# Performance work log

Measured on AMD Instinct MI355X. Metric: run time of the kernel, lower is better.

Reference implementation:

```python
import jax, jax.numpy as jnp
import numpy as np
import math

D_MODEL = 1024
NUM_HEADS = 16
HEAD_DIM = D_MODEL // NUM_HEADS
THETA = 10000.0
B, S = 2, 2048


def apply_rope(x, pos, theta=THETA):
    # x: [..., S, D]; pos: [S] int. Rotates consecutive (even, odd) pairs.
    d = x.shape[-1]
    inv_freq = theta ** (-jnp.arange(0, d, 2, dtype=jnp.float32) / d)  # [d/2]
    ang = pos.astype(jnp.float32)[:, None] * inv_freq[None, :]          # [S, d/2]
    cos, sin = jnp.cos(ang), jnp.sin(ang)
    xe = x[..., 0::2]
    xo = x[..., 1::2]
    re = xe * cos - xo * sin
    ro = xe * sin + xo * cos
    return jnp.stack([re, ro], axis=-1).reshape(x.shape)


def setup_inputs() -> dict:
    key = jax.random.key(0)
    ks = jax.random.split(key, 5)
    scale = 1.0 / math.sqrt(D_MODEL)
    return {
        "in_features": jax.random.normal(ks[0], (B, S, D_MODEL), dtype=jnp.float32),
        "token_positions": jnp.arange(S, dtype=jnp.int32),
        "wq": jax.random.normal(ks[1], (D_MODEL, D_MODEL), dtype=jnp.float32) * scale,
        "wk": jax.random.normal(ks[2], (D_MODEL, D_MODEL), dtype=jnp.float32) * scale,
        "wv": jax.random.normal(ks[3], (D_MODEL, D_MODEL), dtype=jnp.float32) * scale,
        "wo": jax.random.normal(ks[4], (D_MODEL, D_MODEL), dtype=jnp.float32) * scale,
    }


def reference(in_features, token_positions, wq, wk, wv, wo):
    x = in_features
    b, s, d = x.shape
    # Linear: y = x @ W.T  (weight stored as [out, in])
    def split_heads(y):
        return y.reshape(b, s, NUM_HEADS, HEAD_DIM).transpose(0, 2, 1, 3)  # [B,H,S,Dh]
    Q = split_heads(x @ wq.T)
    K = split_heads(x @ wk.T)
    V = split_heads(x @ wv.T)
    Q = apply_rope(Q, token_positions)
    K = apply_rope(K, token_positions)
    scores = jnp.einsum('bhqd,bhkd->bhqk', Q, K) / math.sqrt(HEAD_DIM)
    causal = jnp.tril(jnp.ones((s, s), dtype=bool))
    scores = jnp.where(causal, scores, -jnp.inf)
    weights = jax.nn.softmax(scores, axis=-1)
    out = jnp.einsum('bhqk,bhkd->bhqd', weights, V)  # [B,H,S,Dh]
    out = out.transpose(0, 2, 1, 3).reshape(b, s, d)
    return out @ wo.T
```

## Files before the change

### kernel.cpp

```cpp
#include <hip/hip_runtime.h>
#include <hip/hip_bf16.h>

typedef __bf16 bf16_t;
typedef __bf16 bf16x8 __attribute__((ext_vector_type(8)));
typedef __bf16 bf16x4 __attribute__((ext_vector_type(4)));
typedef float  f32x4  __attribute__((ext_vector_type(4)));
typedef float  f32x16 __attribute__((ext_vector_type(16)));
typedef unsigned int u32;
typedef unsigned int u32x2v __attribute__((ext_vector_type(2)));
typedef unsigned int u32x4v __attribute__((ext_vector_type(4)));

#define D_MODEL   1024
#define NQKV      3072
#define NUM_HEADS 16
#define HEAD_DIM  64
#define SEQ       2048
#define BATCH     2
#define NTOK      4096
#define SM_SCALE_LOG2E 0.18033688011112042f
#define NEG_BIG  (-3.0e38f)

__device__ __forceinline__ int swz128(int row, int bytecol) {
  return row*128 + ((((bytecol>>4) ^ (row&7))<<4) | (bytecol & 15));
}

__device__ __forceinline__ void gload16(const void* g, void* l) {
  __builtin_amdgcn_global_load_lds((const __attribute__((address_space(1))) u32*)g,
                                   (__attribute__((address_space(3))) u32*)l, 16, 0, 0);
}

__device__ __forceinline__ u32 cvtpk_bf16(float a, float b) {
  u32 r;
  asm("v_cvt_pk_bf16_f32 %0, %1, %2" : "=v"(r) : "v"(a), "v"(b));
  return r;
}

__device__ __forceinline__ void plswap(u32 &a, u32 &b) {
#if __has_builtin(__builtin_amdgcn_permlane32_swap)
  u32x2v r = __builtin_amdgcn_permlane32_swap(a, b, false, false);
  a = r[0]; b = r[1];
#else
  u32 xa = __shfl_xor((unsigned)a, 32, 64);
  u32 xb = __shfl_xor((unsigned)b, 32, 64);
  bool hi = (threadIdx.x & 32) != 0;
  a = hi ? xb : a;
  b = hi ? b : xa;
#endif
}

__device__ const unsigned char slot_order96[96] = {
  30,31,88,90,92,93,94,95,
  28,29,80,82,84,85,86,87,89,91,
  26,27,72,74,76,77,78,79,81,83,
  24,25,64,66,68,69,70,71,73,75,
  22,23,56,58,60,61,62,63,65,67,
  20,21,48,50,52,53,54,55,57,59,
  18,19,40,42,44,45,46,47,49,51,
  16,17,32,34,36,37,38,39,41,43,
  14,15,33,35,
  12,13, 10,11, 8,9, 6,7, 4,5, 2,3, 0,1
};

__global__ void cvt_x(const float* __restrict__ in, bf16_t* __restrict__ out) {
  int i = (blockIdx.x*256 + threadIdx.x)*4;
  float4 v = *reinterpret_cast<const float4*>(in + i);
  bf16x4 o; o[0]=(bf16_t)v.x; o[1]=(bf16_t)v.y; o[2]=(bf16_t)v.z; o[3]=(bf16_t)v.w;
  *reinterpret_cast<bf16x4*>(out + i) = o;
}

__global__ void cvt_w(const float* __restrict__ wq, const float* __restrict__ wk,
                      const float* __restrict__ wv, const float* __restrict__ wo,
                      bf16_t* __restrict__ wqkv, bf16_t* __restrict__ wob) {
  const int NW = D_MODEL*D_MODEL;
  int i = (blockIdx.x*256 + threadIdx.x)*4;
  float4 v;
  if      (i <   NW) v = *reinterpret_cast<const float4*>(wq + i);
  else if (i < 2*NW) v = *reinterpret_cast<const float4*>(wk + i - NW);
  else if (i < 3*NW) v = *reinterpret_cast<const float4*>(wv + i - 2*NW);
  else               v = *reinterpret_cast<const float4*>(wo + i - 3*NW);
  bf16x4 o; o[0]=(bf16_t)v.x; o[1]=(bf16_t)v.y; o[2]=(bf16_t)v.z; o[3]=(bf16_t)v.w;
  bf16_t* dst = (i < 3*NW) ? (wqkv + i) : (wob + i - 3*NW);
  *reinterpret_cast<bf16x4*>(dst) = o;
}

__global__ void rope_qk(bf16_t* __restrict__ QKV, const int* __restrict__ pos) {
  int i = blockIdx.x*256 + threadIdx.x;
  int j = i & 31;
  int hp = (i >> 5) & 15;
  int t  = i >> 9;
  float ang = (float)pos[t & (SEQ-1)] * exp2f(-(float)j * (13.287712379549449f/32.0f));
  float sv, cv; sincosf(ang, &sv, &cv);
  size_t base = (size_t)t*NQKV + hp*64 + 2*j;
  float xe = (float)QKV[base], xo = (float)QKV[base+1];
  QKV[base]   = (bf16_t)((xe*cv - xo*sv)*SM_SCALE_LOG2E);
  QKV[base+1] = (bf16_t)((xe*sv + xo*cv)*SM_SCALE_LOG2E);
  xe = (float)QKV[base+1024]; xo = (float)QKV[base+1025];
  QKV[base+1024] = (bf16_t)(xe*cv - xo*sv);
  QKV[base+1025] = (bf16_t)(xe*sv + xo*cv);
}

template<typename OutT, bool QKV>
__global__ __launch_bounds__(256, 1) void gemm8(const bf16_t* __restrict__ A,
                                                const bf16_t* __restrict__ B,
                                                OutT* __restrict__ C,
                                                bf16_t* __restrict__ Vt,
                                                int M, int N, int K) {
  __shared__ __align__(16) char lds[4][32768];
  int tid = threadIdx.x;
  int n0 = blockIdx.x*128, m0 = blockIdx.y*128;
  int wid = tid>>6, lane = tid&63;
  int wr = wid>>1, wc = wid&1;
  int lr = lane&15, lg = lane>>4;

  const int nT = K >> 6;

  int srow = tid >> 3;
  int sc8  = (tid & 7) ^ (srow & 7);
  const bf16_t* ga = A + (size_t)(m0 + srow)*K + sc8*8;
  const bf16_t* gb = B + (size_t)(n0 + srow)*K + sc8*8;

  f32x4 acc[4][4];
  #pragma unroll
  for (int a=0;a<4;a++)
    #pragma unroll
    for (int b=0;b<4;b++) acc[a][b] = (f32x4){0.f,0.f,0.f,0.f};

  auto stage = [&](int t) {
    char* s = lds[t&3];
    int k0 = t << 6;
    #pragma unroll
    for (int g=0; g<4; g++)
      gload16(ga + (size_t)(g*32)*K + k0, s + g*4096 + tid*16);
    #pragma unroll
    for (int g=0; g<4; g++)
      gload16(gb + (size_t)(g*32)*K + k0, s + 16384 + g*4096 + tid*16);
  };

  stage(0);
  if (nT > 1) stage(1);
  asm volatile("s_waitcnt vmcnt(8)" ::: "memory");
  __builtin_amdgcn_sched_barrier(0);
  __builtin_amdgcn_s_barrier();

  for (int t = 0; t < nT; ++t) {
    char* sA = lds[t&3];
    char* sB = sA + 16384;

    bf16x8 bq[4][2], aq[2][2];
    #pragma unroll
    for (int ni=0; ni<4; ni++)
      #pragma unroll
      for (int ks=0; ks<2; ks++)
        bq[ni][ks] = *reinterpret_cast<const bf16x8*>(sB + swz128(wc*64+ni*16+lr, ks*64+lg*16));
    #pragma unroll
    for (int mi=0; mi<2; mi++)
      #pragma unroll
      for (int ks=0; ks<2; ks++)
        aq[mi][ks] = *reinterpret_cast<const bf16x8*>(sA + swz128(wr*64+mi*16+lr, ks*64+lg*16));
    if (t + 2 < nT) stage(t + 2);
    asm volatile("s_waitcnt lgkmcnt(0)" ::: "memory");
    __builtin_amdgcn_sched_barrier(0);
    __builtin_amdgcn_s_setprio(1);
    #pragma unroll
    for (int mi=0; mi<2; mi++)
      #pragma unroll
      for (int ni=0; ni<4; ni++)
        #pragma unroll
        for (int ks=0; ks<2; ks++)
          acc[mi][ni] = __builtin_amdgcn_mfma_f32_16x16x32_bf16(aq[mi][ks], bq[ni][ks], acc[mi][ni], 0, 0, 0);
    __builtin_amdgcn_s_setprio(0);
    __builtin_amdgcn_s_barrier();

    bf16x8 aq2[2][2];
    #pragma unroll
    for (int mi=0; mi<2; mi++)
      #pragma unroll
      for (int ks=0; ks<2; ks++)
        aq2[mi][ks] = *reinterpret_cast<const bf16x8*>(sA + swz128(wr*64+(mi+2)*16+lr, ks*64+lg*16));
    asm volatile("s_waitcnt lgkmcnt(0)" ::: "memory");
    __builtin_amdgcn_sched_barrier(0);
    __builtin_amdgcn_s_setprio(1);
    #pragma unroll
    for (int mi=0; mi<2; mi++)
      #pragma unroll
      for (int ni=0; ni<4; ni++)
        #pragma unroll
        for (int ks=0; ks<2; ks++)
          acc[mi+2][ni] = __builtin_amdgcn_mfma_f32_16x16x32_bf16(aq2[mi][ks], bq[ni][ks], acc[mi+2][ni], 0, 0, 0);
    __builtin_amdgcn_s_setprio(0);
    if (t + 2 < nT)      { asm volatile("s_waitcnt vmcnt(8)" ::: "memory"); }
    else if (t + 1 < nT) { asm volatile("s_waitcnt vmcnt(0)" ::: "memory"); }
    __builtin_amdgcn_sched_barrier(0);
    __builtin_amdgcn_s_barrier();
  }

  if (!QKV || n0 < 2*D_MODEL) {
    #pragma unroll
    for (int mi=0;mi<4;mi++)
      #pragma unroll
      for (int ni=0;ni<4;ni++)
        #pragma unroll
        for (int r=0;r<4;r++) {
          int m = m0 + wr*64 + mi*16 + lg*4 + r;
          int n = n0 + wc*64 + ni*16 + lr;
          C[(size_t)m*N + n] = (OutT)acc[mi][ni][r];
        }
  } else {
    #pragma unroll
    for (int mi=0;mi<4;mi++)
      #pragma unroll
      for (int ni=0;ni<4;ni++)
        #pragma unroll
        for (int r=0;r<4;r++) {
          int m = m0 + wr*64 + mi*16 + lg*4 + r;
          int nl = n0 + wc*64 + ni*16 + lr - 2*D_MODEL;
          int h = nl >> 6, d = nl & 63;
          int bb = m >> 11, s = m & (SEQ-1);
          Vt[(((size_t)(bb*16 + h)*64 + d) << 11) + s] = (bf16_t)acc[mi][ni][r];
        }
  }
}

__global__ __launch_bounds__(64, 3) void attn10(const bf16_t* __restrict__ QKV,
                                                const bf16_t* __restrict__ Vt,
                                                bf16_t* __restrict__ pO,
                                                float2* __restrict__ pML) {
  __shared__ __align__(16) char sK[64*128];

  int bh = blockIdx.x;
  int b = bh >> 4, h = bh & 15;
  int lane = threadIdx.x & 63;
  int q32 = lane & 31, hi = lane >> 5;
  int rsub = lane >> 3, sg = (lane & 7) ^ rsub;

  int s = slot_order96[blockIdx.y];
  int qw, t0, t1;
  if (s < 32) { qw = s; t0 = 0; t1 = (s >> 1) + 1; }
  else {
    int e = s - 32;
    qw = 32 + (e >> 1);
    int nt = (qw >> 1) + 1, h0 = (nt + 1) >> 1;
    t0 = (e & 1) ? h0 : 0;
    t1 = (e & 1) ? nt : h0;
  }
  int qt   = qw >> 1;
  int slot = bh*96 + s;
  int qg   = qw*32 + q32;

  bf16x8 qf[4];
  const bf16_t* qrow = QKV + (size_t)(b*SEQ + qw*32 + q32)*NQKV + h*64 + hi*8;
  #pragma unroll
  for (int d=0; d<4; d++) qf[d] = *reinterpret_cast<const bf16x8*>(qrow + d*16);

  const bf16_t* kgb = QKV + D_MODEL + ((size_t)(b*SEQ) + rsub)*NQKV + h*64 + sg*8;
  const bf16_t* vg0 = Vt + (size_t)bh*64*SEQ + (size_t)q32*SEQ + hi*8;
  const bf16_t* vg1 = vg0 + (size_t)32*SEQ;

  auto stageK = [&](int t) {
    const bf16_t* src = kgb + (size_t)t*64*NQKV;
    #pragma unroll
    for (int c=0;c<8;c++)
      gload16(src + (size_t)(8*c)*NQKV, sK + c*1024 + lane*16);
  };

  f32x16 O0 = (f32x16)0.0f, O1 = (f32x16)0.0f;
  float mrun = NEG_BIG, lrun = 0.f;

  stageK(t0);
  asm volatile("s_waitcnt vmcnt(0)" ::: "memory");
  __builtin_amdgcn_sched_barrier(0);

  for (int ti = t0; ti < t1; ++ti) {
    bf16x8 k0f[4], k1f[4];
    #pragma unroll
    for (int ds=0; ds<4; ds++) {
      k0f[ds] = *reinterpret_cast<const bf16x8*>(sK + swz128(q32,    ds*32 + hi*16));
      k1f[ds] = *reinterpret_cast<const bf16x8*>(sK + swz128(32+q32, ds*32 + hi*16));
    }
    bf16x8 v0f[4], v1f[4];
    #pragma unroll
    for (int ks=0; ks<4; ks++) {
      v0f[ks] = *reinterpret_cast<const bf16x8*>(vg0 + ti*64 + ks*16);
      v1f[ks] = *reinterpret_cast<const bf16x8*>(vg1 + ti*64 + ks*16);
    }
    asm volatile("s_waitcnt lgkmcnt(0)" ::: "memory");
    __builtin_amdgcn_sched_barrier(0);
    if (ti + 1 < t1) stageK(ti + 1);

    f32x16 p0 = (f32x16)0.0f, p1 = (f32x16)0.0f;
    __builtin_amdgcn_s_setprio(1);
    #pragma unroll
    for (int ds=0; ds<4; ds++) {
      p0 = __builtin_amdgcn_mfma_f32_32x32x16_bf16(k0f[ds], qf[ds], p0, 0, 0, 0);
      p1 = __builtin_amdgcn_mfma_f32_32x32x16_bf16(k1f[ds], qf[ds], p1, 0, 0, 0);
    }
    __builtin_amdgcn_s_setprio(0);

    if (ti == qt) {
      #pragma unroll
      for (int r=0; r<16; r++) {
        int kg = ti*64 + (r&3) + 8*(r>>2) + 4*hi;
        if (kg      > qg) p0[r] = NEG_BIG;
        if (kg + 32 > qg) p1[r] = NEG_BIG;
      }
    }

    float mx[8];
    #pragma unroll
    for (int r=0;r<8;r++) mx[r] = fmaxf(fmaxf(p0[r],p0[r+8]), fmaxf(p1[r],p1[r+8]));
    #pragma unroll
    for (int st=4; st>0; st>>=1)
      #pragma unroll
      for (int r=0;r<st;r++) mx[r] = fmaxf(mx[r], mx[r+st]);
    float mt = fmaxf(mx[0], __shfl_xor(mx[0], 32, 64));

    if (!__all(mt <= mrun + 8.0f)) {
      float mnew  = fmaxf(mrun, mt);
      float alpha = exp2f(mrun - mnew);
      lrun *= alpha;
      O0 *= alpha; O1 *= alpha;
      mrun = mnew;
    }
    #pragma unroll
    for (int r=0; r<16; r++) {
      p0[r] = exp2f(p0[r] - mrun);
      p1[r] = exp2f(p1[r] - mrun);
    }
    float sx[8];
    #pragma unroll
    for (int r=0;r<8;r++) sx[r] = (p0[r]+p0[r+8]) + (p1[r]+p1[r+8]);
    #pragma unroll
    for (int st=4; st>0; st>>=1)
      #pragma unroll
      for (int r=0;r<st;r++) sx[r] += sx[r+st];
    lrun += sx[0] + __shfl_xor(sx[0], 32, 64);

    u32 pk0[8], pk1[8];
    #pragma unroll
    for (int i2=0; i2<8; i2++) {
      pk0[i2] = cvtpk_bf16(p0[2*i2], p0[2*i2+1]);
      pk1[i2] = cvtpk_bf16(p1[2*i2], p1[2*i2+1]);
    }
    plswap(pk0[0], pk0[2]); plswap(pk0[1], pk0[3]);
    plswap(pk0[4], pk0[6]); plswap(pk0[5], pk0[7]);
    plswap(pk1[0], pk1[2]); plswap(pk1[1], pk1[3]);
    plswap(pk1[4], pk1[6]); plswap(pk1[5], pk1[7]);

    bf16x8 pa[4];
    pa[0] = __builtin_bit_cast(bf16x8, (u32x4v){pk0[0],pk0[1],pk0[2],pk0[3]});
    pa[1] = __builtin_bit_cast(bf16x8, (u32x4v){pk0[4],pk0[5],pk0[6],pk0[7]});
    pa[2] = __builtin_bit_cast(bf16x8, (u32x4v){pk1[0],pk1[1],pk1[2],pk1[3]});
    pa[3] = __builtin_bit_cast(bf16x8, (u32x4v){pk1[4],pk1[5],pk1[6],pk1[7]});

    __builtin_amdgcn_s_setprio(1);
    #pragma unroll
    for (int ks=0; ks<4; ks++) {
      O0 = __builtin_amdgcn_mfma_f32_32x32x16_bf16(v0f[ks], pa[ks], O0, 0, 0, 0);
      O1 = __builtin_amdgcn_mfma_f32_32x32x16_bf16(v1f[ks], pa[ks], O1, 0, 0, 0);
    }
    __builtin_amdgcn_s_setprio(0);

    if (ti + 1 < t1) {
      asm volatile("s_waitcnt vmcnt(0)" ::: "memory");
      __builtin_amdgcn_sched_barrier(0);
    }
  }

  bf16_t* prow = pO + ((size_t)slot*2048 + q32*64);
  #pragma unroll
  for (int rg=0; rg<4; rg++) {
    int d0 = 8*rg + 4*hi;
    u32 a0 = cvtpk_bf16(O0[4*rg],   O0[4*rg+1]);
    u32 a1 = cvtpk_bf16(O0[4*rg+2], O0[4*rg+3]);
    *reinterpret_cast<u32x2v*>(prow + d0) = (u32x2v){a0, a1};
    u32 b0 = cvtpk_bf16(O1[4*rg],   O1[4*rg+1]);
    u32 b1 = cvtpk_bf16(O1[4*rg+2], O1[4*rg+3]);
    *reinterpret_cast<u32x2v*>(prow + 32 + d0) = (u32x2v){b0, b1};
  }
  if (hi == 0)
    pML[slot*32 + q32] = make_float2(mrun, lrun);
}

__global__ __launch_bounds__(128) void combine(const bf16_t* __restrict__ pO,
                                               const float2* __restrict__ pML,
                                               bf16_t* __restrict__ Of) {
  int qw = blockIdx.x, bh = blockIdx.y;
  int b = bh >> 4, h = bh & 15;
  int t = threadIdx.x;
  int q = t >> 2, d0 = (t & 3) * 16;
  bf16x8 r0, r1;
  if (qw < 32) {
    int slot = bh*96 + qw;
    float2 ml = pML[slot*32 + q];
    float inv = 1.0f / ml.y;
    const bf16x8* src = reinterpret_cast<const bf16x8*>(pO + (size_t)slot*2048 + q*64 + d0);
    bf16x8 o0 = src[0], o1 = src[1];
    #pragma unroll
    for (int i=0;i<8;i++) {
      r0[i] = (bf16_t)((float)o0[i]*inv);
      r1[i] = (bf16_t)((float)o1[i]*inv);
    }
  } else {
    int s0 = bh*96 + 32 + (qw-32)*2;
    float2 mlA = pML[s0*32 + q];
    float2 mlB = pML[(s0+1)*32 + q];
    float m  = fmaxf(mlA.x, mlB.x);
    float a0 = exp2f(mlA.x - m), a1 = exp2f(mlB.x - m);
    float inv = 1.0f / (a0*mlA.y + a1*mlB.y);
    a0 *= inv; a1 *= inv;
    const bf16x8* sA = reinterpret_cast<const bf16x8*>(pO + (size_t)s0*2048 + q*64 + d0);
    const bf16x8* sB = reinterpret_cast<const bf16x8*>(pO + (size_t)(s0+1)*2048 + q*64 + d0);
    bf16x8 oa0 = sA[0], oa1 = sA[1], ob0 = sB[0], ob1 = sB[1];
    #pragma unroll
    for (int i=0;i<8;i++) {
      r0[i] = (bf16_t)(a0*(float)oa0[i] + a1*(float)ob0[i]);
      r1[i] = (bf16_t)(a0*(float)oa1[i] + a1*(float)ob1[i]);
    }
  }
  bf16x8* dst = reinterpret_cast<bf16x8*>(Of + ((size_t)(b*SEQ) + qw*32 + q)*D_MODEL + h*64 + d0);
  dst[0] = r0; dst[1] = r1;
}

extern "C" void kernel_launch(void* const* d_in, const int* in_sizes, int n_in,
                              void* d_out, int out_size, void* d_ws, size_t ws_size,
                              hipStream_t stream) {
  const float* x   = (const float*)d_in[0];
  const int*   pos = (const int*)  d_in[1];
  const float* wq  = (const float*)d_in[2];
  const float* wk  = (const float*)d_in[3];
  const float* wv  = (const float*)d_in[4];
  const float* wo  = (const float*)d_in[5];
  float* out = (float*)d_out;

  char* ws = (char*)d_ws;
  bf16_t* xb   = (bf16_t*)(ws);
  bf16_t* wqkv = (bf16_t*)(ws + ( 8u<<20));
  bf16_t* wob  = (bf16_t*)(ws + (14u<<20));
  bf16_t* QKV  = (bf16_t*)(ws + (16u<<20));
  bf16_t* Vtb  = (bf16_t*)(ws + (40u<<20));
  bf16_t* pO   = (bf16_t*)(ws);
  float2* pML  = (float2*)(ws + (13u<<20));
  bf16_t* Of   = (bf16_t*)(ws + (40u<<20));

  cvt_x<<<NTOK*D_MODEL/1024, 256, 0, stream>>>(x, xb);
  cvt_w<<<4*D_MODEL*D_MODEL/1024, 256, 0, stream>>>(wq, wk, wv, wo, wqkv, wob);

  dim3 gqkv(NQKV/128, NTOK/128);
  gemm8<bf16_t, true><<<gqkv, 256, 0, stream>>>(xb, wqkv, QKV, Vtb, NTOK, NQKV, D_MODEL);

  rope_qk<<<NTOK*NUM_HEADS*32/256, 256, 0, stream>>>(QKV, pos);

  dim3 gattn(32, 96);
  attn10<<<gattn, 64, 0, stream>>>(QKV, Vtb, pO, pML);

  dim3 gcomb(64, 32);
  combine<<<gcomb, 128, 0, stream>>>(pO, pML, Of);

  dim3 gout(D_MODEL/128, NTOK/128);
  gemm8<float, false><<<gout, 256, 0, stream>>>(Of, wob, out, nullptr, NTOK, D_MODEL, D_MODEL);
}
```

Baseline: 136.9 us.

## Double KV tile to 128 keys and stage V through swizzled LDS

```diff
diff --git a/kernel.cpp b/kernel.cpp
--- a/kernel.cpp
+++ b/kernel.cpp
@@ -22,6 +22,9 @@
 
 __device__ __forceinline__ int swz128(int row, int bytecol) {
   return row*128 + ((((bytecol>>4) ^ (row&7))<<4) | (bytecol & 15));
+}
+__device__ __forceinline__ int swz256(int row, int bytecol) {
+  return row*256 + ((((bytecol>>4) ^ (row&15))<<4) | (bytecol & 15));
 }
 
 __device__ __forceinline__ void gload16(const void* g, void* l) {
@@ -49,16 +52,12 @@
 }
 
 __device__ const unsigned char slot_order96[96] = {
-  30,31,88,90,92,93,94,95,
-  28,29,80,82,84,85,86,87,89,91,
-  26,27,72,74,76,77,78,79,81,83,
-  24,25,64,66,68,69,70,71,73,75,
-  22,23,56,58,60,61,62,63,65,67,
-  20,21,48,50,52,53,54,55,57,59,
-  18,19,40,42,44,45,46,47,49,51,
-  16,17,32,34,36,37,38,39,41,43,
-  14,15,33,35,
-  12,13, 10,11, 8,9, 6,7, 4,5, 2,3, 0,1
+  28,29,30,31, 80,82,84,86, 88,89,90,91,92,93,94,95,
+  24,25,26,27, 64,66,68,70, 72,73,74,75,76,77,78,79, 81,83,85,87,
+  20,21,22,23, 48,50,52,54, 56,57,58,59,60,61,62,63, 65,67,69,71,
+  16,17,18,19, 32,34,36,38, 40,41,42,43,44,45,46,47, 49,51,53,55,
+  12,13,14,15, 33,35,37,39,
+  8,9,10,11, 4,5,6,7, 0,1,2,3
 };
 
 __global__ void cvt_x(const float* __restrict__ in, bf16_t* __restrict__ out) {
@@ -221,11 +220,12 @@
   }
 }
 
-__global__ __launch_bounds__(64, 3) void attn10(const bf16_t* __restrict__ QKV,
+__global__ __launch_bounds__(64, 2) void attn12(const bf16_t* __restrict__ QKV,
                                                 const bf16_t* __restrict__ Vt,
                                                 bf16_t* __restrict__ pO,
                                                 float2* __restrict__ pML) {
-  __shared__ __align__(16) char sK[64*128];
+  __shared__ __align__(16) char sK[128*128];
+  __shared__ __align__(16) char sV[64*256];
 
   int bh = blockIdx.x;
   int b = bh >> 4, h = bh & 15;
@@ -235,15 +235,15 @@
 
   int s = slot_order96[blockIdx.y];
   int qw, t0, t1;
-  if (s < 32) { qw = s; t0 = 0; t1 = (s >> 1) + 1; }
+  if (s < 32) { qw = s; t0 = 0; t1 = (s >> 2) + 1; }
   else {
     int e = s - 32;
     qw = 32 + (e >> 1);
-    int nt = (qw >> 1) + 1, h0 = (nt + 1) >> 1;
+    int nt = (qw >> 2) + 1, h0 = (nt + 1) >> 1;
     t0 = (e & 1) ? h0 : 0;
     t1 = (e & 1) ? nt : h0;
   }
-  int qt   = qw >> 1;
+  int qt   = qw >> 2;
   int slot = bh*96 + s;
   int qg   = qw*32 + q32;
 
@@ -253,61 +253,70 @@
   for (int d=0; d<4; d++) qf[d] = *reinterpret_cast<const bf16x8*>(qrow + d*16);
 
   const bf16_t* kgb = QKV + D_MODEL + ((size_t)(b*SEQ) + rsub)*NQKV + h*64 + sg*8;
-  const bf16_t* vg0 = Vt + (size_t)bh*64*SEQ + (size_t)q32*SEQ + hi*8;
-  const bf16_t* vg1 = vg0 + (size_t)32*SEQ;
+  const bf16_t* Vb  = Vt + (size_t)bh*64*SEQ;
 
   auto stageK = [&](int t) {
-    const bf16_t* src = kgb + (size_t)t*64*NQKV;
-    #pragma unroll
-    for (int c=0;c<8;c++)
+    const bf16_t* src = kgb + (size_t)t*128*NQKV;
+    #pragma unroll
+    for (int c=0;c<16;c++)
       gload16(src + (size_t)(8*c)*NQKV, sK + c*1024 + lane*16);
   };
+  auto stageV = [&](int t) {
+    #pragma unroll
+    for (int c=0;c<16;c++) {
+      int row = 4*c + (lane>>4);
+      int sgv = (lane&15) ^ (row & 15);
+      gload16(Vb + (size_t)row*SEQ + t*128 + sgv*8, sV + c*1024 + lane*16);
+    }
+  };
 
   f32x16 O0 = (f32x16)0.0f, O1 = (f32x16)0.0f;
   float mrun = NEG_BIG, lrun = 0.f;
 
-  stageK(t0);
-  asm volatile("s_waitcnt vmcnt(0)" ::: "memory");
-  __builtin_amdgcn_sched_barrier(0);
+  stageK(t0); stageV(t0);
 
   for (int ti = t0; ti < t1; ++ti) {
-    bf16x8 k0f[4], k1f[4];
-    #pragma unroll
-    for (int ds=0; ds<4; ds++) {
-      k0f[ds] = *reinterpret_cast<const bf16x8*>(sK + swz128(q32,    ds*32 + hi*16));
-      k1f[ds] = *reinterpret_cast<const bf16x8*>(sK + swz128(32+q32, ds*32 + hi*16));
-    }
-    bf16x8 v0f[4], v1f[4];
-    #pragma unroll
-    for (int ks=0; ks<4; ks++) {
-      v0f[ks] = *reinterpret_cast<const bf16x8*>(vg0 + ti*64 + ks*16);
-      v1f[ks] = *reinterpret_cast<const bf16x8*>(vg1 + ti*64 + ks*16);
-    }
+    asm volatile("s_waitcnt vmcnt(16)" ::: "memory");
+    __builtin_amdgcn_sched_barrier(0);
+
+    f32x16 p0 = (f32x16)0.0f, p1 = (f32x16)0.0f;
+    f32x16 p2 = (f32x16)0.0f, p3 = (f32x16)0.0f;
+    __builtin_amdgcn_s_setprio(1);
+    #pragma unroll
+    for (int g=0; g<4; g++) {
+      bf16x8 kf[4];
+      #pragma unroll
+      for (int ds=0; ds<4; ds++)
+        kf[ds] = *reinterpret_cast<const bf16x8*>(sK + swz128(g*32 + q32, ds*32 + hi*16));
+      #pragma unroll
+      for (int ds=0; ds<4; ds++) {
+        if (g == 0) p0 = __builtin_amdgcn_mfma_f32_32x32x16_bf16(kf[ds], qf[ds], p0, 0, 0, 0);
+        if (g == 1) p1 = __builtin_amdgcn_mfma_f32_32x32x16_bf16(kf[ds], qf[ds], p1, 0, 0, 0);
+        if (g == 2) p2 = __builtin_amdgcn_mfma_f32_32x32x16_bf16(kf[ds], qf[ds], p2, 0, 0, 0);
+        if (g == 3) p3 = __builtin_amdgcn_mfma_f32_32x32x16_bf16(kf[ds], qf[ds], p3, 0, 0, 0);
+      }
+    }
+    __builtin_amdgcn_s_setprio(0);
     asm volatile("s_waitcnt lgkmcnt(0)" ::: "memory");
     __builtin_amdgcn_sched_barrier(0);
     if (ti + 1 < t1) stageK(ti + 1);
 
-    f32x16 p0 = (f32x16)0.0f, p1 = (f32x16)0.0f;
-    __builtin_amdgcn_s_setprio(1);
-    #pragma unroll
-    for (int ds=0; ds<4; ds++) {
-      p0 = __builtin_amdgcn_mfma_f32_32x32x16_bf16(k0f[ds], qf[ds], p0, 0, 0, 0);
-      p1 = __builtin_amdgcn_mfma_f32_32x32x16_bf16(k1f[ds], qf[ds], p1, 0, 0, 0);
-    }
-    __builtin_amdgcn_s_setprio(0);
-
     if (ti == qt) {
       #pragma unroll
       for (int r=0; r<16; r++) {
-        int kg = ti*64 + (r&3) + 8*(r>>2) + 4*hi;
-        if (kg      > qg) p0[r] = NEG_BIG;
-        if (kg + 32 > qg) p1[r] = NEG_BIG;
+        int kg = ti*128 + (r&3) + 8*(r>>2) + 4*hi;
+        if (kg       > qg) p0[r] = NEG_BIG;
+        if (kg + 32  > qg) p1[r] = NEG_BIG;
+        if (kg + 64  > qg) p2[r] = NEG_BIG;
+        if (kg + 96  > qg) p3[r] = NEG_BIG;
       }
     }
 
     float mx[8];
     #pragma unroll
-    for (int r=0;r<8;r++) mx[r] = fmaxf(fmaxf(p0[r],p0[r+8]), fmaxf(p1[r],p1[r+8]));
+    for (int r=0;r<8;r++)
+      mx[r] = fmaxf(fmaxf(fmaxf(p0[r],p0[r+8]), fmaxf(p1[r],p1[r+8])),
+                    fmaxf(fmaxf(p2[r],p2[r+8]), fmaxf(p3[r],p3[r+8])));
     #pragma unroll
     for (int st=4; st>0; st>>=1)
       #pragma unroll
@@ -325,45 +334,56 @@
     for (int r=0; r<16; r++) {
       p0[r] = exp2f(p0[r] - mrun);
       p1[r] = exp2f(p1[r] - mrun);
+      p2[r] = exp2f(p2[r] - mrun);
+      p3[r] = exp2f(p3[r] - mrun);
     }
     float sx[8];
     #pragma unroll
-    for (int r=0;r<8;r++) sx[r] = (p0[r]+p0[r+8]) + (p1[r]+p1[r+8]);
+    for (int r=0;r<8;r++)
+      sx[r] = ((p0[r]+p0[r+8]) + (p1[r]+p1[r+8])) + ((p2[r]+p2[r+8]) + (p3[r]+p3[r+8]));
     #pragma unroll
     for (int st=4; st>0; st>>=1)
       #pragma unroll
       for (int r=0;r<st;r++) sx[r] += sx[r+st];
     lrun += sx[0] + __shfl_xor(sx[0], 32, 64);
 
-    u32 pk0[8], pk1[8];
-    #pragma unroll
-    for (int i2=0; i2<8; i2++) {
-      pk0[i2] = cvtpk_bf16(p0[2*i2], p0[2*i2+1]);
-      pk1[i2] = cvtpk_bf16(p1[2*i2], p1[2*i2+1]);
-    }
-    plswap(pk0[0], pk0[2]); plswap(pk0[1], pk0[3]);
-    plswap(pk0[4], pk0[6]); plswap(pk0[5], pk0[7]);
-    plswap(pk1[0], pk1[2]); plswap(pk1[1], pk1[3]);
-    plswap(pk1[4], pk1[6]); plswap(pk1[5], pk1[7]);
-
-    bf16x8 pa[4];
-    pa[0] = __builtin_bit_cast(bf16x8, (u32x4v){pk0[0],pk0[1],pk0[2],pk0[3]});
-    pa[1] = __builtin_bit_cast(bf16x8, (u32x4v){pk0[4],pk0[5],pk0[6],pk0[7]});
-    pa[2] = __builtin_bit_cast(bf16x8, (u32x4v){pk1[0],pk1[1],pk1[2],pk1[3]});
-    pa[3] = __builtin_bit_cast(bf16x8, (u32x4v){pk1[4],pk1[5],pk1[6],pk1[7]});
+    bf16x8 pa[8];
+    #pragma unroll
+    for (int g=0; g<4; g++) {
+      u32 pk[8];
+      #pragma unroll
+      for (int i2=0; i2<8; i2++) {
+        float a = (g==0)?p0[2*i2]:(g==1)?p1[2*i2]:(g==2)?p2[2*i2]:p3[2*i2];
+        float c = (g==0)?p0[2*i2+1]:(g==1)?p1[2*i2+1]:(g==2)?p2[2*i2+1]:p3[2*i2+1];
+        pk[i2] = cvtpk_bf16(a, c);
+      }
+      plswap(pk[0], pk[2]); plswap(pk[1], pk[3]);
+      plswap(pk[4], pk[6]); plswap(pk[5], pk[7]);
+      pa[2*g]   = __builtin_bit_cast(bf16x8, (u32x4v){pk[0],pk[1],pk[2],pk[3]});
+      pa[2*g+1] = __builtin_bit_cast(bf16x8, (u32x4v){pk[4],pk[5],pk[6],pk[7]});
+    }
+
+    if (ti + 1 < t1) { asm volatile("s_waitcnt vmcnt(16)" ::: "memory"); }
+    else             { asm volatile("s_waitcnt vmcnt(0)"  ::: "memory"); }
+    __builtin_amdgcn_sched_barrier(0);
+
+    bf16x8 v0f[8], v1f[8];
+    #pragma unroll
+    for (int ks=0; ks<8; ks++) {
+      v0f[ks] = *reinterpret_cast<const bf16x8*>(sV + swz256(q32,    ks*32 + hi*16));
+      v1f[ks] = *reinterpret_cast<const bf16x8*>(sV + swz256(32+q32, ks*32 + hi*16));
+    }
+    asm volatile("s_waitcnt lgkmcnt(0)" ::: "memory");
+    __builtin_amdgcn_sched_barrier(0);
+    if (ti + 1 < t1) stageV(ti + 1);
 
     __builtin_amdgcn_s_setprio(1);
     #pragma unroll
-    for (int ks=0; ks<4; ks++) {
+    for (int ks=0; ks<8; ks++) {
       O0 = __builtin_amdgcn_mfma_f32_32x32x16_bf16(v0f[ks], pa[ks], O0, 0, 0, 0);
       O1 = __builtin_amdgcn_mfma_f32_32x32x16_bf16(v1f[ks], pa[ks], O1, 0, 0, 0);
     }
     __builtin_amdgcn_s_setprio(0);
-
-    if (ti + 1 < t1) {
-      asm volatile("s_waitcnt vmcnt(0)" ::: "memory");
-      __builtin_amdgcn_sched_barrier(0);
-    }
   }
 
   bf16_t* prow = pO + ((size_t)slot*2048 + q32*64);
@@ -451,7 +471,7 @@
   rope_qk<<<NTOK*NUM_HEADS*32/256, 256, 0, stream>>>(QKV, pos);
 
   dim3 gattn(32, 96);
-  attn10<<<gattn, 64, 0, stream>>>(QKV, Vtb, pO, pML);
+  attn12<<<gattn, 64, 0, stream>>>(QKV, Vtb, pO, pML);
 
   dim3 gcomb(64, 32);
   combine<<<gcomb, 128, 0, stream>>>(pO, pML, Of);
```

Measured after the change: 150.5 us. 9.9% more time.
